# Kernel optimization log

Measured on AMD Instinct MI355X. Metric: run time of the kernel, lower is better.

## Reference

```python
import jax, jax.numpy as jnp
import numpy as np

VAR0, VAR1 = 0.1, 0.2
THRESH = 0.5
NEG_POS = 3
NEG_INF = -1e30


def point_form(b):
    # (cx,cy,w,h) -> (x1,y1,x2,y2)
    return jnp.concatenate([b[..., :2] - b[..., 2:] * 0.5,
                            b[..., :2] + b[..., 2:] * 0.5], -1)


def iou(a, b):
    # a: [G,4], b: [A,4], both xyxy -> [G,A]
    tl = jnp.maximum(a[:, None, :2], b[None, :, :2])
    br = jnp.minimum(a[:, None, 2:], b[None, :, 2:])
    wh = jnp.clip(br - tl, 0.0)
    inter = wh[..., 0] * wh[..., 1]
    area_a = (a[:, 2] - a[:, 0]) * (a[:, 3] - a[:, 1])
    area_b = (b[:, 2] - b[:, 0]) * (b[:, 3] - b[:, 1])
    return inter / (area_a[:, None] + area_b[None, :] - inter)


def encode_single(gt_boxes, gt_labels, anchors):
    # gt_boxes [G,4] xyxy, gt_labels [G], anchors [A,4] cxcywh
    ov = iou(gt_boxes, point_form(anchors))            # [G,A]
    best_prior_idx = jnp.argmax(ov, axis=1)            # [G] guaranteed match
    best_truth_ov = jnp.max(ov, axis=0)                # [A]
    best_truth_idx = jnp.argmax(ov, axis=0)            # [A]
    G = gt_boxes.shape[0]
    best_truth_ov = best_truth_ov.at[best_prior_idx].set(2.0)
    best_truth_idx = best_truth_idx.at[best_prior_idx].set(jnp.arange(G))
    matches = gt_boxes[best_truth_idx]                 # [A,4]
    conf = jnp.where(best_truth_ov < THRESH, 0, gt_labels[best_truth_idx] + 1)
    m_cxcy = (matches[:, :2] + matches[:, 2:]) * 0.5
    m_wh = matches[:, 2:] - matches[:, :2]
    g_cxcy = (m_cxcy - anchors[:, :2]) / (VAR0 * anchors[:, 2:])
    g_wh = jnp.log(m_wh / anchors[:, 2:]) / VAR1
    return conf, jnp.concatenate([g_cxcy, g_wh], -1)


def smooth_l1(d):
    ad = jnp.abs(d)
    return jnp.where(ad < 1.0, 0.5 * d * d, ad - 0.5)


def ssd_guarantee_loss(pred_conf, pred_loc, anchors_b, gt_boxes, gt_labels):
    # anchors_b: per-image anchors [B,A,4] (cxcywh)
    conf_t, loc_t = jax.vmap(encode_single)(gt_boxes, gt_labels, anchors_b)
    loc_t = jax.lax.stop_gradient(loc_t)               # loc_t.detach() in torch
    pos = conf_t > 0                                   # [B,A]
    N = jnp.sum(pos).astype(pred_loc.dtype)
    loc_loss = jnp.sum(jnp.where(pos[..., None], smooth_l1(pred_loc - loc_t), 0.0))
    logp = jax.nn.log_softmax(pred_conf, axis=-1)
    ce = -jnp.take_along_axis(logp, conf_t[..., None], axis=-1)[..., 0]  # [B,A]
    A = pred_conf.shape[1]
    pos_num = jnp.sum(pos, axis=1)                     # [B]
    neg_num = jnp.maximum(10, jnp.minimum(pos_num * NEG_POS, A - pos_num))
    neg_ce = jnp.where(conf_t == 0, ce, NEG_INF)
    neg_sorted = -jnp.sort(-neg_ce, axis=1)            # descending hard-negative sort
    rank = jnp.arange(A)
    take = (rank[None, :] < neg_num[:, None]) & (neg_sorted > 0.5 * NEG_INF)
    class_loss = (jnp.sum(jnp.where(pos, ce, 0.0))
                  + jnp.sum(jnp.where(take, neg_sorted, 0.0))) / N
    return class_loss, loc_loss / N, N


def decode(loc, anchors):
    # loc [B,A,4], anchors [A,4] cxcywh -> refined anchors [B,A,4] cxcywh
    cxcy = anchors[None, :, :2] + loc[..., :2] * VAR0 * anchors[None, :, 2:]
    wh = anchors[None, :, 2:] * jnp.exp(loc[..., 2:] * VAR1)
    return jnp.concatenate([cxcy, wh], -1)


def setup_inputs() -> dict:
    key = jax.random.key(0)
    ks = jax.random.split(key, 10)
    B, A, C, G = 32, 16320, 81, 32
    objectness = jax.random.normal(ks[0], (B, A, 2), jnp.float32)
    refine_loc = 0.1 * jax.random.normal(ks[1], (B, A, 4), jnp.float32)
    pred_conf = jax.random.normal(ks[2], (B, A, C), jnp.float32)
    pred_loc = 0.1 * jax.random.normal(ks[3], (B, A, 4), jnp.float32)
    # anchors: valid normalized cxcywh
    a_cxcy = 0.05 + 0.9 * jax.random.uniform(ks[4], (1, A, 2), jnp.float32)
    a_wh = 0.02 + 0.23 * jax.random.uniform(ks[5], (1, A, 2), jnp.float32)
    anchors = jnp.concatenate([a_cxcy, a_wh], -1)
    # gt boxes: valid xyxy in [0,1]
    g_cxcy = 0.2 + 0.6 * jax.random.uniform(ks[6], (B, G, 2), jnp.float32)
    g_wh = 0.05 + 0.25 * jax.random.uniform(ks[7], (B, G, 2), jnp.float32)
    gt_boxes = jnp.clip(jnp.concatenate([g_cxcy - g_wh * 0.5, g_cxcy + g_wh * 0.5], -1), 0.0, 1.0)
    gt_labels = jax.random.randint(ks[8], (B, G), 0, C - 1, jnp.int32)
    return {"objectness": objectness, "refine_loc": refine_loc, "pred_conf": pred_conf,
            "pred_loc": pred_loc, "anchors": anchors, "gt_boxes": gt_boxes,
            "gt_labels": gt_labels}


def reference(objectness, refine_loc, pred_conf, pred_loc, anchors, gt_boxes, gt_labels):
    a0 = anchors[0]                                    # [A,4]
    B = pred_conf.shape[0]
    anchors_b = jnp.broadcast_to(a0, (B,) + a0.shape)
    # ARM: binary objectness, labels zeroed
    arm_cls, arm_loc, _ = ssd_guarantee_loss(objectness, refine_loc, anchors_b,
                                             gt_boxes, jnp.zeros_like(gt_labels))
    # ODM: match against per-image refined anchors
    refined = decode(refine_loc, a0)
    odm_cls, odm_loc, _ = ssd_guarantee_loss(pred_conf, pred_loc, refined,
                                             gt_boxes, gt_labels)
    total = arm_cls + arm_loc + odm_cls + odm_loc
    return (total, odm_cls, odm_loc, arm_cls, arm_loc)
```

## Files before the change

### kernel.cpp

```cpp
#include <hip/hip_runtime.h>
#include <hip/hip_bf16.h>

constexpr int NB = 32;
constexpr int NA = 16320;
constexpr int NG = 32;
constexpr int NC = 81;
constexpr int ARM_GRID = 1024;
constexpr int ODM_GRID = 2048;

__device__ __forceinline__ float sl1(float d) {
    float ad = fabsf(d);
    return ad < 1.f ? 0.5f * d * d : ad - 0.5f;
}

__global__ __launch_bounds__(256) void k_decode(
    const float* __restrict__ anchors,
    const float* __restrict__ refine_loc,
    float4* __restrict__ pf,
    float* __restrict__ parea)
{
    int idx = blockIdx.x * 256 + threadIdx.x;
    if (idx >= (NB + 1) * NA) return;
    int row = idx / NA;
    int a = idx - row * NA;
    float4 an = *(const float4*)&anchors[(size_t)a * 4];
    float acx = an.x, acy = an.y, aw = an.z, ah = an.w;
    if (row > 0) {
        int b = row - 1;
        float4 rl = *(const float4*)&refine_loc[((size_t)b * NA + a) * 4];
        acx += rl.x * 0.1f * aw;
        acy += rl.y * 0.1f * ah;
        aw *= __expf(rl.z * 0.2f);
        ah *= __expf(rl.w * 0.2f);
    }
    float4 o;
    o.x = acx - aw * 0.5f; o.y = acy - ah * 0.5f;
    o.z = acx + aw * 0.5f; o.w = acy + ah * 0.5f;
    pf[idx] = o;
    parea[idx] = (o.z - o.x) * (o.w - o.y);
}

__global__ __launch_bounds__(256) void k_match_a(
    const float4* __restrict__ pf,
    const float* __restrict__ parea,
    const float* __restrict__ gt_boxes,
    float* __restrict__ ws_ov,
    unsigned char* __restrict__ ws_idx)
{
    int row = blockIdx.x >> 6;
    int chunk = blockIdx.x & 63;
    int lossId = row >> 5, b = row & 31;
    int tid = threadIdx.x;
    __shared__ float4 s_gt[NG];
    __shared__ float s_ga[NG];
    if (tid < NG) {
        float4 g = *(const float4*)&gt_boxes[(size_t)(b * NG + tid) * 4];
        s_gt[tid] = g;
        s_ga[tid] = (g.z - g.x) * (g.w - g.y);
    }
    __syncthreads();
    int a = chunk * 256 + tid;
    if (a >= NA) return;
    int prow = lossId ? (1 + b) : 0;
    float4 A = pf[(size_t)prow * NA + a];
    float aarea = parea[(size_t)prow * NA + a];
    float best = -1.f; int bg = 0;
    #pragma unroll 4
    for (int g = 0; g < NG; g++) {
        float4 G = s_gt[g];
        float tlx = fmaxf(G.x, A.x);
        float tly = fmaxf(G.y, A.y);
        float brx = fminf(G.z, A.z);
        float bry = fminf(G.w, A.w);
        float w = brx - tlx; w = w > 0.f ? w : 0.f;
        float h = bry - tly; h = h > 0.f ? h : 0.f;
        float inter = w * h;
        float uni = s_ga[g] + aarea - inter;
        float ov = inter * __builtin_amdgcn_rcpf(uni);
        if (ov > best) { best = ov; bg = g; }
    }
    size_t sec = (size_t)row * NA;
    ws_ov[sec + a] = best;
    ws_idx[sec + a] = (unsigned char)bg;
}

__global__ __launch_bounds__(256) void k_match_g(
    const float4* __restrict__ pf,
    const float* __restrict__ parea,
    const float* __restrict__ gt_boxes,
    unsigned long long* __restrict__ ws_best)
{
    int blk = blockIdx.x;
    int row = blk >> 4;
    int gpair = blk & 15;
    int lossId = row >> 5, b = row & 31;
    int g0 = gpair * 2;
    float4 G0 = *(const float4*)&gt_boxes[(size_t)(b * NG + g0) * 4];
    float4 G1 = *(const float4*)&gt_boxes[(size_t)(b * NG + g0 + 1) * 4];
    float ga0 = (G0.z - G0.x) * (G0.w - G0.y);
    float ga1 = (G1.z - G1.x) * (G1.w - G1.y);
    int prow = lossId ? (1 + b) : 0;
    const float4* P = pf + (size_t)prow * NA;
    const float* PA = parea + (size_t)prow * NA;
    unsigned long long k0 = 0ull, k1 = 0ull;
    for (int a = threadIdx.x; a < NA; a += 256) {
        float4 A = P[a];
        float aa = PA[a];
        unsigned inv_a = 0xFFFFFFFFu - (unsigned)a;
        {
            float tlx = fmaxf(G0.x, A.x), tly = fmaxf(G0.y, A.y);
            float brx = fminf(G0.z, A.z), bry = fminf(G0.w, A.w);
            float w = brx - tlx; w = w > 0.f ? w : 0.f;
            float h = bry - tly; h = h > 0.f ? h : 0.f;
            float inter = w * h;
            float ov = inter * __builtin_amdgcn_rcpf(ga0 + aa - inter);
            unsigned long long key = ((unsigned long long)__float_as_uint(ov) << 32) | inv_a;
            k0 = key > k0 ? key : k0;
        }
        {
            float tlx = fmaxf(G1.x, A.x), tly = fmaxf(G1.y, A.y);
            float brx = fminf(G1.z, A.z), bry = fminf(G1.w, A.w);
            float w = brx - tlx; w = w > 0.f ? w : 0.f;
            float h = bry - tly; h = h > 0.f ? h : 0.f;
            float inter = w * h;
            float ov = inter * __builtin_amdgcn_rcpf(ga1 + aa - inter);
            unsigned long long key = ((unsigned long long)__float_as_uint(ov) << 32) | inv_a;
            k1 = key > k1 ? key : k1;
        }
    }
    #pragma unroll
    for (int o = 32; o > 0; o >>= 1) {
        unsigned long long t0 = __shfl_down(k0, o);
        unsigned long long t1 = __shfl_down(k1, o);
        k0 = t0 > k0 ? t0 : k0;
        k1 = t1 > k1 ? t1 : k1;
    }
    __shared__ unsigned long long s0[4], s1[4];
    int w = threadIdx.x >> 6;
    if ((threadIdx.x & 63) == 0) { s0[w] = k0; s1[w] = k1; }
    __syncthreads();
    if (threadIdx.x == 0) {
        unsigned long long m0 = s0[0], m1 = s1[0];
        for (int i = 1; i < 4; i++) {
            m0 = s0[i] > m0 ? s0[i] : m0;
            m1 = s1[i] > m1 ? s1[i] : m1;
        }
        ws_best[(size_t)row * NG + g0] = m0;
        ws_best[(size_t)row * NG + g0 + 1] = m1;
    }
}

__global__ __launch_bounds__(256) void k_conf(
    const int* __restrict__ gt_labels,
    const unsigned long long* __restrict__ ws_best,
    const float* __restrict__ ws_ov,
    const unsigned char* __restrict__ ws_idx,
    int* __restrict__ match,
    int* __restrict__ pos_cnt)
{
    int row = blockIdx.x >> 3;
    int chunk = blockIdx.x & 7;
    int lossId = row >> 5, b = row & 31;
    int tid = threadIdx.x;
    __shared__ int s_oa[NG];
    __shared__ int s_lab[NG];
    __shared__ unsigned s_mask[512];
    for (int i = tid; i < 512; i += 256) s_mask[i] = 0u;
    __syncthreads();
    if (tid < NG) {
        s_lab[tid] = lossId ? gt_labels[b * NG + tid] : 0;
        unsigned a = 0xFFFFFFFFu - (unsigned)(ws_best[(size_t)row * NG + tid] & 0xFFFFFFFFull);
        s_oa[tid] = (int)a;
        atomicOr(&s_mask[a >> 5], 1u << (a & 31));
    }
    __syncthreads();
    size_t sec = (size_t)row * NA;
    int base = chunk * 2040;
    int cnt = 0;
    for (int a = base + tid; a < base + 2040; a += 256) {
        float ov = ws_ov[sec + a];
        int g = ws_idx[sec + a];
        if (s_mask[a >> 5] & (1u << (a & 31))) {
            for (int j = NG - 1; j >= 0; j--)
                if (s_oa[j] == a) { g = j; ov = 2.0f; break; }
        }
        int conf = (ov < 0.5f) ? 0 : (s_lab[g] + 1);
        match[sec + a] = conf | (g << 16);
        cnt += (conf > 0);
    }
    #pragma unroll
    for (int o = 32; o > 0; o >>= 1) cnt += __shfl_down(cnt, o);
    __shared__ int s_c[4];
    if ((tid & 63) == 0) s_c[tid >> 6] = cnt;
    __syncthreads();
    if (tid == 0) pos_cnt[blockIdx.x] = s_c[0] + s_c[1] + s_c[2] + s_c[3];
}

__device__ __forceinline__ void block_reduce2_store(float v0, float v1, float2* dst) {
    #pragma unroll
    for (int o = 32; o > 0; o >>= 1) { v0 += __shfl_down(v0, o); v1 += __shfl_down(v1, o); }
    __shared__ float s0[4], s1[4];
    int w = threadIdx.x >> 6;
    if ((threadIdx.x & 63) == 0) { s0[w] = v0; s1[w] = v1; }
    __syncthreads();
    if (threadIdx.x == 0) {
        float t0 = 0.f, t1 = 0.f;
        #pragma unroll
        for (int i = 0; i < 4; i++) { t0 += s0[i]; t1 += s1[i]; }
        *dst = make_float2(t0, t1);
    }
}

__global__ __launch_bounds__(256) void k_arm_loss(
    const float* __restrict__ objectness,
    const float* __restrict__ refine_loc,
    const float* __restrict__ anchors,
    const float* __restrict__ gt_boxes,
    const int* __restrict__ match,
    float* __restrict__ negce,
    float2* __restrict__ partial)
{
    float pce = 0.f, ploc = 0.f;
    for (int idx = blockIdx.x * 256 + threadIdx.x; idx < NB * NA; idx += ARM_GRID * 256) {
        int b = idx / NA, a = idx - b * NA;
        float2 x = *(const float2*)&objectness[(size_t)idx * 2];
        float mx = fmaxf(x.x, x.y);
        float s = __expf(x.x - mx) + __expf(x.y - mx);
        float lse = mx + __logf(s);
        int m = match[idx]; int conf = m & 0xFFFF; int g = m >> 16;
        float ce = lse - (conf ? x.y : x.x);
        if (conf > 0) {
            pce += ce;
            negce[idx] = 0.f;
            float4 an = *(const float4*)&anchors[(size_t)a * 4];
            const float* gb = &gt_boxes[(size_t)(b * NG + g) * 4];
            float mcx = (gb[0] + gb[2]) * 0.5f, mcy = (gb[1] + gb[3]) * 0.5f;
            float mw = gb[2] - gb[0], mh = gb[3] - gb[1];
            float t0 = (mcx - an.x) / (0.1f * an.z);
            float t1 = (mcy - an.y) / (0.1f * an.w);
            float t2 = __logf(mw / an.z) / 0.2f;
            float t3 = __logf(mh / an.w) / 0.2f;
            float4 pl = *(const float4*)&refine_loc[(size_t)idx * 4];
            ploc += sl1(pl.x - t0) + sl1(pl.y - t1) + sl1(pl.z - t2) + sl1(pl.w - t3);
        } else {
            negce[idx] = ce;
        }
    }
    block_reduce2_store(pce, ploc, &partial[blockIdx.x]);
}

__device__ __forceinline__ void odm_anchor(
    int idx, const float* x, float x80, int m, int sub,
    const float* __restrict__ anchors, const float* __restrict__ refine_loc,
    const float* __restrict__ gt_boxes, const float* __restrict__ pred_loc,
    float* __restrict__ negce, float& pce, float& ploc)
{
    int conf = m & 0xFFFF; int g = m >> 16;
    float mx = x80;
    #pragma unroll
    for (int j = 0; j < 10; j++) mx = fmaxf(mx, x[j]);
    mx = fmaxf(mx, __shfl_xor(mx, 1));
    mx = fmaxf(mx, __shfl_xor(mx, 2));
    mx = fmaxf(mx, __shfl_xor(mx, 4));
    float s = (sub == 0) ? __expf(x80 - mx) : 0.f;
    float sel = (sub == 0 && conf == 80) ? x80 : 0.f;
    #pragma unroll
    for (int j = 0; j < 10; j++) {
        s += __expf(x[j] - mx);
        sel += (sub + 8 * j == conf) ? x[j] : 0.f;
    }
    s += __shfl_xor(s, 1);   sel += __shfl_xor(sel, 1);
    s += __shfl_xor(s, 2);   sel += __shfl_xor(sel, 2);
    s += __shfl_xor(s, 4);   sel += __shfl_xor(sel, 4);
    float ce = mx + __logf(s) - sel;
    if (sub == 0) {
        if (conf > 0) {
            pce += ce;
            negce[idx] = 0.f;
            int b = idx / NA, a = idx - b * NA;
            float4 an = *(const float4*)&anchors[(size_t)a * 4];
            float4 rl = *(const float4*)&refine_loc[(size_t)idx * 4];
            float acx = an.x + rl.x * 0.1f * an.z;
            float acy = an.y + rl.y * 0.1f * an.w;
            float aw = an.z * __expf(rl.z * 0.2f);
            float ah = an.w * __expf(rl.w * 0.2f);
            const float* gb = &gt_boxes[(size_t)(b * NG + g) * 4];
            float mcx = (gb[0] + gb[2]) * 0.5f, mcy = (gb[1] + gb[3]) * 0.5f;
            float mw = gb[2] - gb[0], mh = gb[3] - gb[1];
            float t0 = (mcx - acx) / (0.1f * aw);
            float t1 = (mcy - acy) / (0.1f * ah);
            float t2 = __logf(mw / aw) / 0.2f;
            float t3 = __logf(mh / ah) / 0.2f;
            float4 pl = *(const float4*)&pred_loc[(size_t)idx * 4];
            ploc += sl1(pl.x - t0) + sl1(pl.y - t1) + sl1(pl.z - t2) + sl1(pl.w - t3);
        } else {
            negce[idx] = ce;
        }
    }
}

__global__ __launch_bounds__(256, 4) void k_odm_loss(
    const float* __restrict__ pred_conf,
    const float* __restrict__ pred_loc,
    const float* __restrict__ anchors,
    const float* __restrict__ refine_loc,
    const float* __restrict__ gt_boxes,
    const int* __restrict__ match,
    float* __restrict__ negce,
    float2* __restrict__ partial)
{
    int lane = threadIdx.x & 63;
    int sub = lane & 7;
    int grp = lane >> 3;
    int wid = blockIdx.x * 4 + (threadIdx.x >> 6);
    const int NWAVE = ODM_GRID * 4;
    const int TOT = NB * NA / 8;
    float pce = 0.f, ploc = 0.f;

    float x[10], x80; int m, idx;
    {
        idx = wid * 8 + grp;
        const float* p = pred_conf + (size_t)idx * NC;
        #pragma unroll
        for (int j = 0; j < 10; j++) x[j] = p[sub + 8 * j];
        x80 = (sub == 0) ? p[80] : -3.0e38f;
        m = match[idx];
    }
    for (int gi = wid; gi < TOT; gi += NWAVE) {
        float y[10], y80 = 0.f; int my = 0, idxy = 0;
        int nx = gi + NWAVE;
        if (nx < TOT) {
            idxy = nx * 8 + grp;
            const float* p = pred_conf + (size_t)idxy * NC;
            #pragma unroll
            for (int j = 0; j < 10; j++) y[j] = p[sub + 8 * j];
            y80 = (sub == 0) ? p[80] : -3.0e38f;
            my = match[idxy];
        }
        odm_anchor(idx, x, x80, m, sub, anchors, refine_loc, gt_boxes, pred_loc,
                   negce, pce, ploc);
        #pragma unroll
        for (int j = 0; j < 10; j++) x[j] = y[j];
        x80 = y80; m = my; idx = idxy;
    }
    block_reduce2_store(pce, ploc, &partial[blockIdx.x]);
}

__global__ __launch_bounds__(256) void k_topk(
    const float* __restrict__ negce,
    const int* __restrict__ pos_cnt,
    float* __restrict__ topk)
{
    int blk = blockIdx.x;
    int tid = threadIdx.x;
    size_t sec = (size_t)blk * NA;
    float v[64];
    #pragma unroll
    for (int q = 0; q < 64; q++) {
        int i = tid + (q << 8);
        v[q] = (i < NA) ? negce[sec + i] : 0.f;
    }
    __shared__ int s_red[4];
    __shared__ float s_redf[4];
    int p = 0;
    #pragma unroll
    for (int j = 0; j < 8; j++) p += pos_cnt[blk * 8 + j];
    int k = p * 3; if (k > NA - p) k = NA - p; if (k < 10) k = 10;

    unsigned lo = 0u, hi = 0x7F800000u;
    while (lo < hi) {
        unsigned mid = (lo + hi) >> 1;
        float fmid = __uint_as_float(mid);
        int c = 0;
        #pragma unroll
        for (int q = 0; q < 64; q++) c += (v[q] > fmid);
        #pragma unroll
        for (int o = 32; o > 0; o >>= 1) c += __shfl_down(c, o);
        if ((tid & 63) == 0) s_red[tid >> 6] = c;
        __syncthreads();
        int total = s_red[0] + s_red[1] + s_red[2] + s_red[3];
        __syncthreads();
        if (total < k) hi = mid; else lo = mid + 1;
    }
    float V = __uint_as_float(lo);
    int c = 0; float sum = 0.f;
    #pragma unroll
    for (int q = 0; q < 64; q++) {
        if (v[q] > V) { c++; sum += v[q]; }
    }
    #pragma unroll
    for (int o = 32; o > 0; o >>= 1) { c += __shfl_down(c, o); sum += __shfl_down(sum, o); }
    if ((tid & 63) == 0) { s_red[tid >> 6] = c; s_redf[tid >> 6] = sum; }
    __syncthreads();
    if (tid == 0) {
        int cg = s_red[0] + s_red[1] + s_red[2] + s_red[3];
        float sg = s_redf[0] + s_redf[1] + s_redf[2] + s_redf[3];
        topk[blk] = sg + (float)(k - cg) * V;
    }
}

__global__ __launch_bounds__(256) void k_final(
    const float2* __restrict__ pArm, const float2* __restrict__ pOdm,
    const int* __restrict__ pos_cnt, const float* __restrict__ topk,
    float* __restrict__ out)
{
    int tid = threadIdx.x;
    float a0 = 0.f, a1 = 0.f, o0 = 0.f, o1 = 0.f;
    for (int i = tid; i < ARM_GRID; i += 256) { float2 v = pArm[i]; a0 += v.x; a1 += v.y; }
    for (int i = tid; i < ODM_GRID; i += 256) { float2 v = pOdm[i]; o0 += v.x; o1 += v.y; }
    float n0 = (float)pos_cnt[tid];
    float n1 = (float)pos_cnt[256 + tid];
    float t0 = (tid < NB) ? topk[tid] : 0.f;
    float t1 = (tid < NB) ? topk[NB + tid] : 0.f;
    #pragma unroll
    for (int o = 32; o > 0; o >>= 1) {
        a0 += __shfl_down(a0, o); a1 += __shfl_down(a1, o);
        o0 += __shfl_down(o0, o); o1 += __shfl_down(o1, o);
        n0 += __shfl_down(n0, o); n1 += __shfl_down(n1, o);
        t0 += __shfl_down(t0, o); t1 += __shfl_down(t1, o);
    }
    __shared__ float s[4][8];
    if ((tid & 63) == 0) {
        int w = tid >> 6;
        s[w][0] = a0; s[w][1] = a1; s[w][2] = o0; s[w][3] = o1;
        s[w][4] = n0; s[w][5] = n1; s[w][6] = t0; s[w][7] = t1;
    }
    __syncthreads();
    if (tid == 0) {
        float armce = 0.f, armloc = 0.f, odmce = 0.f, odmloc = 0.f;
        float N0 = 0.f, N1 = 0.f, tk0 = 0.f, tk1 = 0.f;
        #pragma unroll
        for (int i = 0; i < 4; i++) {
            armce += s[i][0]; armloc += s[i][1]; odmce += s[i][2]; odmloc += s[i][3];
            N0 += s[i][4]; N1 += s[i][5]; tk0 += s[i][6]; tk1 += s[i][7];
        }
        float cls0 = (armce + tk0) / N0, loc0 = armloc / N0;
        float cls1 = (odmce + tk1) / N1, loc1 = odmloc / N1;
        out[0] = cls0 + loc0 + cls1 + loc1;
        out[1] = cls1;
        out[2] = loc1;
        out[3] = cls0;
        out[4] = loc0;
    }
}

extern "C" void kernel_launch(void* const* d_in, const int* in_sizes, int n_in,
                              void* d_out, int out_size, void* d_ws, size_t ws_size,
                              hipStream_t stream) {
    const float* objectness = (const float*)d_in[0];
    const float* refine_loc = (const float*)d_in[1];
    const float* pred_conf  = (const float*)d_in[2];
    const float* pred_loc   = (const float*)d_in[3];
    const float* anchors    = (const float*)d_in[4];
    const float* gt_boxes   = (const float*)d_in[5];
    const int*   gt_labels  = (const int*)d_in[6];

    char* w = (char*)d_ws;
    size_t off = 0;
    int* pos_cnt = (int*)(w + off); off += 512 * sizeof(int);
    float* topk = (float*)(w + off); off += 64 * sizeof(float);
    off = (off + 15) & ~(size_t)15;
    float2* pArm = (float2*)(w + off); off += (size_t)ARM_GRID * 8;
    float2* pOdm = (float2*)(w + off); off += (size_t)ODM_GRID * 8;
    unsigned long long* ws_best = (unsigned long long*)(w + off);
    off += (size_t)2 * NB * NG * 8;
    off = (off + 15) & ~(size_t)15;
    float4* pf = (float4*)(w + off); off += (size_t)(NB + 1) * NA * 16;
    float* parea = (float*)(w + off); off += (size_t)(NB + 1) * NA * 4;
    float* ws_ov = (float*)(w + off); off += (size_t)2 * NB * NA * 4;
    unsigned char* ws_idx = (unsigned char*)(w + off); off += (size_t)2 * NB * NA;
    off = (off + 15) & ~(size_t)15;
    int* match = (int*)(w + off); off += (size_t)2 * NB * NA * 4;
    float* negce = (float*)(w + off); off += (size_t)2 * NB * NA * 4;

    k_decode<<<((NB + 1) * NA + 255) / 256, 256, 0, stream>>>(anchors, refine_loc, pf, parea);
    k_match_a<<<64 * 64, 256, 0, stream>>>(pf, parea, gt_boxes, ws_ov, ws_idx);
    k_match_g<<<64 * 16, 256, 0, stream>>>(pf, parea, gt_boxes, ws_best);
    k_conf<<<64 * 8, 256, 0, stream>>>(gt_labels, ws_best, ws_ov, ws_idx, match, pos_cnt);
    k_arm_loss<<<ARM_GRID, 256, 0, stream>>>(objectness, refine_loc, anchors,
                                             gt_boxes, match, negce, pArm);
    k_odm_loss<<<ODM_GRID, 256, 0, stream>>>(pred_conf, pred_loc, anchors, refine_loc,
                                             gt_boxes, match + (size_t)NB * NA,
                                             negce + (size_t)NB * NA, pOdm);
    k_topk<<<2 * NB, 256, 0, stream>>>(negce, pos_cnt, topk);
    k_final<<<1, 256, 0, stream>>>(pArm, pOdm, pos_cnt, topk, (float*)d_out);
}
```

Before: 137.8 us.

## Fuse decode, per-anchor and per-GT matching, and ARM loss into fewer kernels

Anchor decoding is folded into the matching kernel, so the decoded box array no longer goes through global memory. The per-GT best-anchor search is computed inside the same kernel with wave shuffles and ballots, writing per-block partial keys that k_conf then reduces. The ARM loss is computed inside k_conf, which removes the separate ARM pass and its re-read of match. This cuts three launches and several global round trips, at the cost of more registers in k_match (a 32-entry array of overlaps plus a 32-way shuffle reduction) and a partial-key buffer.

```diff
diff --git a/kernel.cpp b/kernel.cpp
--- a/kernel.cpp
+++ b/kernel.cpp
@@ -5,7 +5,6 @@
 constexpr int NA = 16320;
 constexpr int NG = 32;
 constexpr int NC = 81;
-constexpr int ARM_GRID = 1024;
 constexpr int ODM_GRID = 2048;
 
 __device__ __forceinline__ float sl1(float d) {
@@ -13,39 +12,17 @@
     return ad < 1.f ? 0.5f * d * d : ad - 0.5f;
 }
 
-__global__ __launch_bounds__(256) void k_decode(
+__device__ __forceinline__ unsigned long long umax64(unsigned long long a, unsigned long long b) {
+    return a > b ? a : b;
+}
+
+__global__ __launch_bounds__(256) void k_match(
     const float* __restrict__ anchors,
     const float* __restrict__ refine_loc,
-    float4* __restrict__ pf,
-    float* __restrict__ parea)
-{
-    int idx = blockIdx.x * 256 + threadIdx.x;
-    if (idx >= (NB + 1) * NA) return;
-    int row = idx / NA;
-    int a = idx - row * NA;
-    float4 an = *(const float4*)&anchors[(size_t)a * 4];
-    float acx = an.x, acy = an.y, aw = an.z, ah = an.w;
-    if (row > 0) {
-        int b = row - 1;
-        float4 rl = *(const float4*)&refine_loc[((size_t)b * NA + a) * 4];
-        acx += rl.x * 0.1f * aw;
-        acy += rl.y * 0.1f * ah;
-        aw *= __expf(rl.z * 0.2f);
-        ah *= __expf(rl.w * 0.2f);
-    }
-    float4 o;
-    o.x = acx - aw * 0.5f; o.y = acy - ah * 0.5f;
-    o.z = acx + aw * 0.5f; o.w = acy + ah * 0.5f;
-    pf[idx] = o;
-    parea[idx] = (o.z - o.x) * (o.w - o.y);
-}
-
-__global__ __launch_bounds__(256) void k_match_a(
-    const float4* __restrict__ pf,
-    const float* __restrict__ parea,
     const float* __restrict__ gt_boxes,
     float* __restrict__ ws_ov,
-    unsigned char* __restrict__ ws_idx)
+    unsigned char* __restrict__ ws_idx,
+    unsigned long long* __restrict__ ws_part)
 {
     int row = blockIdx.x >> 6;
     int chunk = blockIdx.x & 63;
@@ -53,6 +30,7 @@
     int tid = threadIdx.x;
     __shared__ float4 s_gt[NG];
     __shared__ float s_ga[NG];
+    __shared__ unsigned long long s_part[4][NG];
     if (tid < NG) {
         float4 g = *(const float4*)&gt_boxes[(size_t)(b * NG + tid) * 4];
         s_gt[tid] = g;
@@ -60,103 +38,84 @@
     }
     __syncthreads();
     int a = chunk * 256 + tid;
-    if (a >= NA) return;
-    int prow = lossId ? (1 + b) : 0;
-    float4 A = pf[(size_t)prow * NA + a];
-    float aarea = parea[(size_t)prow * NA + a];
+    bool valid = a < NA;
+    int al = valid ? a : NA - 1;
+    float4 an = *(const float4*)&anchors[(size_t)al * 4];
+    float acx = an.x, acy = an.y, aw = an.z, ah = an.w;
+    if (lossId) {
+        float4 rl = *(const float4*)&refine_loc[((size_t)b * NA + al) * 4];
+        acx += rl.x * 0.1f * aw;
+        acy += rl.y * 0.1f * ah;
+        aw *= __expf(rl.z * 0.2f);
+        ah *= __expf(rl.w * 0.2f);
+    }
+    float ax1 = acx - aw * 0.5f, ay1 = acy - ah * 0.5f;
+    float ax2 = acx + aw * 0.5f, ay2 = acy + ah * 0.5f;
+    float aarea = (ax2 - ax1) * (ay2 - ay1);
+
+    float ovg[NG];
     float best = -1.f; int bg = 0;
-    #pragma unroll 4
+    #pragma unroll
     for (int g = 0; g < NG; g++) {
         float4 G = s_gt[g];
-        float tlx = fmaxf(G.x, A.x);
-        float tly = fmaxf(G.y, A.y);
-        float brx = fminf(G.z, A.z);
-        float bry = fminf(G.w, A.w);
+        float tlx = fmaxf(G.x, ax1);
+        float tly = fmaxf(G.y, ay1);
+        float brx = fminf(G.z, ax2);
+        float bry = fminf(G.w, ay2);
         float w = brx - tlx; w = w > 0.f ? w : 0.f;
         float h = bry - tly; h = h > 0.f ? h : 0.f;
         float inter = w * h;
         float uni = s_ga[g] + aarea - inter;
         float ov = inter * __builtin_amdgcn_rcpf(uni);
+        if (!valid) ov = 0.f;
+        ovg[g] = ov;
         if (ov > best) { best = ov; bg = g; }
     }
-    size_t sec = (size_t)row * NA;
-    ws_ov[sec + a] = best;
-    ws_idx[sec + a] = (unsigned char)bg;
-}
-
-__global__ __launch_bounds__(256) void k_match_g(
-    const float4* __restrict__ pf,
-    const float* __restrict__ parea,
-    const float* __restrict__ gt_boxes,
-    unsigned long long* __restrict__ ws_best)
-{
-    int blk = blockIdx.x;
-    int row = blk >> 4;
-    int gpair = blk & 15;
-    int lossId = row >> 5, b = row & 31;
-    int g0 = gpair * 2;
-    float4 G0 = *(const float4*)&gt_boxes[(size_t)(b * NG + g0) * 4];
-    float4 G1 = *(const float4*)&gt_boxes[(size_t)(b * NG + g0 + 1) * 4];
-    float ga0 = (G0.z - G0.x) * (G0.w - G0.y);
-    float ga1 = (G1.z - G1.x) * (G1.w - G1.y);
-    int prow = lossId ? (1 + b) : 0;
-    const float4* P = pf + (size_t)prow * NA;
-    const float* PA = parea + (size_t)prow * NA;
-    unsigned long long k0 = 0ull, k1 = 0ull;
-    for (int a = threadIdx.x; a < NA; a += 256) {
-        float4 A = P[a];
-        float aa = PA[a];
-        unsigned inv_a = 0xFFFFFFFFu - (unsigned)a;
-        {
-            float tlx = fmaxf(G0.x, A.x), tly = fmaxf(G0.y, A.y);
-            float brx = fminf(G0.z, A.z), bry = fminf(G0.w, A.w);
-            float w = brx - tlx; w = w > 0.f ? w : 0.f;
-            float h = bry - tly; h = h > 0.f ? h : 0.f;
-            float inter = w * h;
-            float ov = inter * __builtin_amdgcn_rcpf(ga0 + aa - inter);
-            unsigned long long key = ((unsigned long long)__float_as_uint(ov) << 32) | inv_a;
-            k0 = key > k0 ? key : k0;
-        }
-        {
-            float tlx = fmaxf(G1.x, A.x), tly = fmaxf(G1.y, A.y);
-            float brx = fminf(G1.z, A.z), bry = fminf(G1.w, A.w);
-            float w = brx - tlx; w = w > 0.f ? w : 0.f;
-            float h = bry - tly; h = h > 0.f ? h : 0.f;
-            float inter = w * h;
-            float ov = inter * __builtin_amdgcn_rcpf(ga1 + aa - inter);
-            unsigned long long key = ((unsigned long long)__float_as_uint(ov) << 32) | inv_a;
-            k1 = key > k1 ? key : k1;
-        }
-    }
-    #pragma unroll
-    for (int o = 32; o > 0; o >>= 1) {
-        unsigned long long t0 = __shfl_down(k0, o);
-        unsigned long long t1 = __shfl_down(k1, o);
-        k0 = t0 > k0 ? t0 : k0;
-        k1 = t1 > k1 ? t1 : k1;
-    }
-    __shared__ unsigned long long s0[4], s1[4];
-    int w = threadIdx.x >> 6;
-    if ((threadIdx.x & 63) == 0) { s0[w] = k0; s1[w] = k1; }
-    __syncthreads();
-    if (threadIdx.x == 0) {
-        unsigned long long m0 = s0[0], m1 = s1[0];
-        for (int i = 1; i < 4; i++) {
-            m0 = s0[i] > m0 ? s0[i] : m0;
-            m1 = s1[i] > m1 ? s1[i] : m1;
-        }
-        ws_best[(size_t)row * NG + g0] = m0;
-        ws_best[(size_t)row * NG + g0 + 1] = m1;
+    if (valid) {
+        size_t sec = (size_t)row * NA;
+        ws_ov[sec + a] = best;
+        ws_idx[sec + a] = (unsigned char)bg;
+    }
+    int lane = tid & 63, wv = tid >> 6;
+    #pragma unroll
+    for (int g = 0; g < NG; g++) {
+        float m = ovg[g];
+        m = fmaxf(m, __shfl_xor(m, 1));
+        m = fmaxf(m, __shfl_xor(m, 2));
+        m = fmaxf(m, __shfl_xor(m, 4));
+        m = fmaxf(m, __shfl_xor(m, 8));
+        m = fmaxf(m, __shfl_xor(m, 16));
+        m = fmaxf(m, __shfl_xor(m, 32));
+        unsigned long long ball = __ballot(ovg[g] == m);
+        int first = __ffsll((long long)ball) - 1;
+        if (lane == 0) {
+            unsigned aw_ = (unsigned)(chunk * 256 + wv * 64 + first);
+            s_part[wv][g] = ((unsigned long long)__float_as_uint(m) << 32)
+                            | (0xFFFFFFFFu - aw_);
+        }
+    }
+    __syncthreads();
+    if (tid < NG) {
+        unsigned long long k = s_part[0][tid];
+        #pragma unroll
+        for (int i = 1; i < 4; i++) k = umax64(k, s_part[i][tid]);
+        ws_part[(size_t)blockIdx.x * NG + tid] = k;
     }
 }
 
 __global__ __launch_bounds__(256) void k_conf(
     const int* __restrict__ gt_labels,
-    const unsigned long long* __restrict__ ws_best,
+    const unsigned long long* __restrict__ ws_part,
     const float* __restrict__ ws_ov,
     const unsigned char* __restrict__ ws_idx,
+    const float* __restrict__ objectness,
+    const float* __restrict__ anchors,
+    const float* __restrict__ gt_boxes,
+    const float* __restrict__ arm_pred,
     int* __restrict__ match,
-    int* __restrict__ pos_cnt)
+    float* __restrict__ negce,
+    int* __restrict__ pos_cnt,
+    float2* __restrict__ pConf)
 {
     int row = blockIdx.x >> 3;
     int chunk = blockIdx.x & 7;
@@ -164,19 +123,33 @@
     int tid = threadIdx.x;
     __shared__ int s_oa[NG];
     __shared__ int s_lab[NG];
+    __shared__ float4 s_gt[NG];
     __shared__ unsigned s_mask[512];
+    __shared__ unsigned long long s_pp[8][NG];
     for (int i = tid; i < 512; i += 256) s_mask[i] = 0u;
+    {
+        int g = tid & 31, s = tid >> 5;
+        unsigned long long k = 0ull;
+        for (int c = s; c < 64; c += 8)
+            k = umax64(k, ws_part[(size_t)(row * 64 + c) * NG + g]);
+        s_pp[s][g] = k;
+    }
     __syncthreads();
     if (tid < NG) {
+        unsigned long long k = s_pp[0][tid];
+        #pragma unroll
+        for (int i = 1; i < 8; i++) k = umax64(k, s_pp[i][tid]);
+        unsigned a = 0xFFFFFFFFu - (unsigned)(k & 0xFFFFFFFFull);
+        s_oa[tid] = (int)a;
         s_lab[tid] = lossId ? gt_labels[b * NG + tid] : 0;
-        unsigned a = 0xFFFFFFFFu - (unsigned)(ws_best[(size_t)row * NG + tid] & 0xFFFFFFFFull);
-        s_oa[tid] = (int)a;
+        s_gt[tid] = *(const float4*)&gt_boxes[(size_t)(b * NG + tid) * 4];
         atomicOr(&s_mask[a >> 5], 1u << (a & 31));
     }
     __syncthreads();
     size_t sec = (size_t)row * NA;
     int base = chunk * 2040;
     int cnt = 0;
+    float pce = 0.f, ploc = 0.f;
     for (int a = base + tid; a < base + 2040; a += 256) {
         float ov = ws_ov[sec + a];
         int g = ws_idx[sec + a];
@@ -185,15 +158,51 @@
                 if (s_oa[j] == a) { g = j; ov = 2.0f; break; }
         }
         int conf = (ov < 0.5f) ? 0 : (s_lab[g] + 1);
-        match[sec + a] = conf | (g << 16);
         cnt += (conf > 0);
-    }
-    #pragma unroll
-    for (int o = 32; o > 0; o >>= 1) cnt += __shfl_down(cnt, o);
+        if (lossId) {
+            match[sec + a] = conf | (g << 16);
+        } else {
+            size_t idx = sec + a;
+            float2 x = *(const float2*)&objectness[idx * 2];
+            float mx = fmaxf(x.x, x.y);
+            float lse = mx + __logf(__expf(x.x - mx) + __expf(x.y - mx));
+            float ce = lse - (conf ? x.y : x.x);
+            if (conf > 0) {
+                pce += ce;
+                negce[idx] = 0.f;
+                float4 an = *(const float4*)&anchors[(size_t)a * 4];
+                float4 G = s_gt[g];
+                float mcx = (G.x + G.z) * 0.5f, mcy = (G.y + G.w) * 0.5f;
+                float mw = G.z - G.x, mh = G.w - G.y;
+                float t0 = (mcx - an.x) / (0.1f * an.z);
+                float t1 = (mcy - an.y) / (0.1f * an.w);
+                float t2 = __logf(mw / an.z) / 0.2f;
+                float t3 = __logf(mh / an.w) / 0.2f;
+                float4 pl = *(const float4*)&arm_pred[idx * 4];
+                ploc += sl1(pl.x - t0) + sl1(pl.y - t1) + sl1(pl.z - t2) + sl1(pl.w - t3);
+            } else {
+                negce[idx] = ce;
+            }
+        }
+    }
+    #pragma unroll
+    for (int o = 32; o > 0; o >>= 1) {
+        cnt += __shfl_down(cnt, o);
+        pce += __shfl_down(pce, o);
+        ploc += __shfl_down(ploc, o);
+    }
     __shared__ int s_c[4];
-    if ((tid & 63) == 0) s_c[tid >> 6] = cnt;
-    __syncthreads();
-    if (tid == 0) pos_cnt[blockIdx.x] = s_c[0] + s_c[1] + s_c[2] + s_c[3];
+    __shared__ float s_p0[4], s_p1[4];
+    if ((tid & 63) == 0) {
+        int w = tid >> 6;
+        s_c[w] = cnt; s_p0[w] = pce; s_p1[w] = ploc;
+    }
+    __syncthreads();
+    if (tid == 0) {
+        pos_cnt[blockIdx.x] = s_c[0] + s_c[1] + s_c[2] + s_c[3];
+        pConf[blockIdx.x] = make_float2(s_p0[0] + s_p0[1] + s_p0[2] + s_p0[3],
+                                        s_p1[0] + s_p1[1] + s_p1[2] + s_p1[3]);
+    }
 }
 
 __device__ __forceinline__ void block_reduce2_store(float v0, float v1, float2* dst) {
@@ -209,44 +218,6 @@
         for (int i = 0; i < 4; i++) { t0 += s0[i]; t1 += s1[i]; }
         *dst = make_float2(t0, t1);
     }
-}
-
-__global__ __launch_bounds__(256) void k_arm_loss(
-    const float* __restrict__ objectness,
-    const float* __restrict__ refine_loc,
-    const float* __restrict__ anchors,
-    const float* __restrict__ gt_boxes,
-    const int* __restrict__ match,
-    float* __restrict__ negce,
-    float2* __restrict__ partial)
-{
-    float pce = 0.f, ploc = 0.f;
-    for (int idx = blockIdx.x * 256 + threadIdx.x; idx < NB * NA; idx += ARM_GRID * 256) {
-        int b = idx / NA, a = idx - b * NA;
-        float2 x = *(const float2*)&objectness[(size_t)idx * 2];
-        float mx = fmaxf(x.x, x.y);
-        float s = __expf(x.x - mx) + __expf(x.y - mx);
-        float lse = mx + __logf(s);
-        int m = match[idx]; int conf = m & 0xFFFF; int g = m >> 16;
-        float ce = lse - (conf ? x.y : x.x);
-        if (conf > 0) {
-            pce += ce;
-            negce[idx] = 0.f;
-            float4 an = *(const float4*)&anchors[(size_t)a * 4];
-            const float* gb = &gt_boxes[(size_t)(b * NG + g) * 4];
-            float mcx = (gb[0] + gb[2]) * 0.5f, mcy = (gb[1] + gb[3]) * 0.5f;
-            float mw = gb[2] - gb[0], mh = gb[3] - gb[1];
-            float t0 = (mcx - an.x) / (0.1f * an.z);
-            float t1 = (mcy - an.y) / (0.1f * an.w);
-            float t2 = __logf(mw / an.z) / 0.2f;
-            float t3 = __logf(mh / an.w) / 0.2f;
-            float4 pl = *(const float4*)&refine_loc[(size_t)idx * 4];
-            ploc += sl1(pl.x - t0) + sl1(pl.y - t1) + sl1(pl.z - t2) + sl1(pl.w - t3);
-        } else {
-            negce[idx] = ce;
-        }
-    }
-    block_reduce2_store(pce, ploc, &partial[blockIdx.x]);
 }
 
 __device__ __forceinline__ void odm_anchor(
@@ -400,13 +371,13 @@
 }
 
 __global__ __launch_bounds__(256) void k_final(
-    const float2* __restrict__ pArm, const float2* __restrict__ pOdm,
+    const float2* __restrict__ pConf, const float2* __restrict__ pOdm,
     const int* __restrict__ pos_cnt, const float* __restrict__ topk,
     float* __restrict__ out)
 {
     int tid = threadIdx.x;
     float a0 = 0.f, a1 = 0.f, o0 = 0.f, o1 = 0.f;
-    for (int i = tid; i < ARM_GRID; i += 256) { float2 v = pArm[i]; a0 += v.x; a1 += v.y; }
+    for (int i = tid; i < 512; i += 256) { float2 v = pConf[i]; a0 += v.x; a1 += v.y; }
     for (int i = tid; i < ODM_GRID; i += 256) { float2 v = pOdm[i]; o0 += v.x; o1 += v.y; }
     float n0 = (float)pos_cnt[tid];
     float n1 = (float)pos_cnt[256 + tid];
@@ -460,28 +431,25 @@
     int* pos_cnt = (int*)(w + off); off += 512 * sizeof(int);
     float* topk = (float*)(w + off); off += 64 * sizeof(float);
     off = (off + 15) & ~(size_t)15;
-    float2* pArm = (float2*)(w + off); off += (size_t)ARM_GRID * 8;
+    float2* pConf = (float2*)(w + off); off += 512 * 8;
     float2* pOdm = (float2*)(w + off); off += (size_t)ODM_GRID * 8;
-    unsigned long long* ws_best = (unsigned long long*)(w + off);
-    off += (size_t)2 * NB * NG * 8;
+    unsigned long long* ws_part = (unsigned long long*)(w + off);
+    off += (size_t)64 * 64 * NG * 8;
     off = (off + 15) & ~(size_t)15;
-    float4* pf = (float4*)(w + off); off += (size_t)(NB + 1) * NA * 16;
-    float* parea = (float*)(w + off); off += (size_t)(NB + 1) * NA * 4;
     float* ws_ov = (float*)(w + off); off += (size_t)2 * NB * NA * 4;
     unsigned char* ws_idx = (unsigned char*)(w + off); off += (size_t)2 * NB * NA;
     off = (off + 15) & ~(size_t)15;
     int* match = (int*)(w + off); off += (size_t)2 * NB * NA * 4;
     float* negce = (float*)(w + off); off += (size_t)2 * NB * NA * 4;
 
-    k_decode<<<((NB + 1) * NA + 255) / 256, 256, 0, stream>>>(anchors, refine_loc, pf, parea);
-    k_match_a<<<64 * 64, 256, 0, stream>>>(pf, parea, gt_boxes, ws_ov, ws_idx);
-    k_match_g<<<64 * 16, 256, 0, stream>>>(pf, parea, gt_boxes, ws_best);
-    k_conf<<<64 * 8, 256, 0, stream>>>(gt_labels, ws_best, ws_ov, ws_idx, match, pos_cnt);
-    k_arm_loss<<<ARM_GRID, 256, 0, stream>>>(objectness, refine_loc, anchors,
-                                             gt_boxes, match, negce, pArm);
+    k_match<<<64 * 64, 256, 0, stream>>>(anchors, refine_loc, gt_boxes,
+                                         ws_ov, ws_idx, ws_part);
+    k_conf<<<64 * 8, 256, 0, stream>>>(gt_labels, ws_part, ws_ov, ws_idx,
+                                       objectness, anchors, gt_boxes, refine_loc,
+                                       match, negce, pos_cnt, pConf);
     k_odm_loss<<<ODM_GRID, 256, 0, stream>>>(pred_conf, pred_loc, anchors, refine_loc,
                                              gt_boxes, match + (size_t)NB * NA,
                                              negce + (size_t)NB * NA, pOdm);
     k_topk<<<2 * NB, 256, 0, stream>>>(negce, pos_cnt, topk);
-    k_final<<<1, 256, 0, stream>>>(pArm, pOdm, pos_cnt, topk, (float*)d_out);
-}
+    k_final<<<1, 256, 0, stream>>>(pConf, pOdm, pos_cnt, topk, (float*)d_out);
+}
```

Result: faster. 134.4 us (-2.5%).
